# Kernel tuning notes

Measured on AMD Instinct MI355X. Metric: run time of the kernel, lower is better.

Reference implementation:

```python
import jax, jax.numpy as jnp
import numpy as np

WS = 7          # window size (square)
SHIFT = 3       # shift size
NH = 8          # num heads
DIM = 256
B, H, W = 32, 56, 56


def _relative_position_index(ws: int) -> np.ndarray:
    coords = np.stack(np.meshgrid(np.arange(ws), np.arange(ws), indexing='ij'))  # (2, ws, ws)
    cf = coords.reshape(2, -1)                                                   # (2, N)
    rel = cf[:, :, None] - cf[:, None, :]                                        # (2, N, N)
    rel = rel.transpose(1, 2, 0).copy()
    rel[:, :, 0] += ws - 1
    rel[:, :, 1] += ws - 1
    rel[:, :, 0] *= 2 * ws - 1
    return rel.sum(-1).reshape(-1).astype(np.int32)                              # (N*N,)


def _shift_mask(h: int, w: int, ws: int, shift: int) -> np.ndarray:
    img = np.zeros((h, w), dtype=np.float32)
    cnt = 0
    for hs in ((0, -ws), (-ws, -shift), (-shift, None)):
        for wsl in ((0, -ws), (-ws, -shift), (-shift, None)):
            img[hs[0]:hs[1], wsl[0]:wsl[1]] = cnt
            cnt += 1
    nwh, nww = h // ws, w // ws
    m = img.reshape(nwh, ws, nww, ws).transpose(0, 2, 1, 3).reshape(nwh * nww, ws * ws)
    am = m[:, None, :] - m[:, :, None]                 # (nW, N, N)
    return np.where(am != 0, np.float32(-100.0), np.float32(0.0))


def setup_inputs() -> dict:
    key = jax.random.key(0)
    ks = jax.random.split(key, 5)
    x = jax.random.normal(ks[0], (B, H, W, DIM), jnp.float32)
    qkv_weight = jax.random.normal(ks[1], (3 * DIM, DIM), jnp.float32) * 0.02
    qkv_bias = jnp.zeros((3 * DIM,), jnp.float32)
    proj_weight = jax.random.normal(ks[2], (DIM, DIM), jnp.float32) * 0.02
    proj_bias = jnp.zeros((DIM,), jnp.float32)
    rel_bias_table = jax.random.normal(ks[3], ((2 * WS - 1) ** 2, NH), jnp.float32) * 0.02
    rel_pos_index = jnp.asarray(_relative_position_index(WS))
    return {
        'x': x, 'qkv_weight': qkv_weight, 'qkv_bias': qkv_bias,
        'proj_weight': proj_weight, 'proj_bias': proj_bias,
        'rel_bias_table': rel_bias_table, 'rel_pos_index': rel_pos_index,
    }


def reference(x, qkv_weight, qkv_bias, proj_weight, proj_bias, rel_bias_table, rel_pos_index):
    b, h, w, c = x.shape
    n = WS * WS
    hd = c // NH
    nwh, nww = h // WS, w // WS
    nw = nwh * nww

    # relative position bias: (1, NH, N, N)
    bias = rel_bias_table[rel_pos_index].reshape(n, n, NH).transpose(2, 0, 1)[None]

    # cyclic shift
    xs = jnp.roll(x, (-SHIFT, -SHIFT), axis=(1, 2))

    # window partition -> (B*nW, N, C)
    xw = xs.reshape(b, nwh, WS, nww, WS, c).transpose(0, 1, 3, 2, 4, 5).reshape(b * nw, n, c)

    qkv = xw @ qkv_weight.T + qkv_bias
    qkv = qkv.reshape(b * nw, n, 3, NH, hd).transpose(2, 0, 3, 1, 4)  # (3, B*nW, NH, N, hd)
    q = qkv[0] * (hd ** -0.5)
    k = qkv[1]
    v = qkv[2]

    attn = jnp.einsum('bhnd,bhmd->bhnm', q, k) + bias                # (B*nW, NH, N, N)

    # shift mask (static)
    amask = jnp.asarray(_shift_mask(h, w, WS, SHIFT))                # (nW, N, N)
    attn = attn.reshape(b, nw, NH, n, n) + amask[None, :, None]
    attn = jax.nn.softmax(attn.reshape(b * nw, NH, n, n), axis=-1)

    out = jnp.einsum('bhnm,bhmd->bhnd', attn, v)                     # (B*nW, NH, N, hd)
    out = out.transpose(0, 2, 1, 3).reshape(b * nw, n, c)
    out = out @ proj_weight.T + proj_bias

    # window reverse + reverse shift
    out = out.reshape(b, nwh, nww, WS, WS, c).transpose(0, 1, 3, 2, 4, 5).reshape(b, h, w, c)
    out = jnp.roll(out, (SHIFT, SHIFT), axis=(1, 2))
    return out
```

## Files before the change

### kernel.cpp

```cpp
#include <hip/hip_runtime.h>
#include <hip/hip_bf16.h>


#define NTOK 49
#define DIM_ 256
#define NH_  8
#define NQKV 196608
#define NPRJ 65536
#define NTABP 131072

#define WSP_B  393216ull
#define TAB_B  524288ull
#define Q_B    1048576ull
#define NEED_BIG 162312448ull
#define NEED_TAB (TAB_B + (unsigned long long)NTABP * 4)

typedef short v8s __attribute__((ext_vector_type(8)));
typedef float v4f __attribute__((ext_vector_type(4)));
typedef float v16f __attribute__((ext_vector_type(16)));

#define MFMA16 __builtin_amdgcn_mfma_f32_16x16x32_bf16
#define MFMA32 __builtin_amdgcn_mfma_f32_32x32x16_bf16
#define LGKM_WAIT() asm volatile("s_waitcnt lgkmcnt(0)" ::: "memory")

static __device__ __forceinline__ v8s zero_v8s() {
    v8s z = {0, 0, 0, 0, 0, 0, 0, 0};
    return z;
}

static __device__ __forceinline__ v16f zero_v16f() {
    v16f z;
    #pragma unroll
    for (int i = 0; i < 16; ++i) z[i] = 0.0f;
    return z;
}

static __device__ __forceinline__ v8s lds_frag(const __hip_bfloat16* p, int row,
                                               int stride, int koff, int nrows) {
    if (row < nrows) return *(const v8s*)(p + row * stride + koff);
    return zero_v8s();
}

static __device__ __forceinline__ v8s cvt8(const float* p) {
    v4f a = *(const v4f*)p;
    v4f b = *(const v4f*)(p + 4);
    union { v8s v; __hip_bfloat16 h[8]; } r;
    r.h[0] = __float2bfloat16(a[0]); r.h[1] = __float2bfloat16(a[1]);
    r.h[2] = __float2bfloat16(a[2]); r.h[3] = __float2bfloat16(a[3]);
    r.h[4] = __float2bfloat16(b[0]); r.h[5] = __float2bfloat16(b[1]);
    r.h[6] = __float2bfloat16(b[2]); r.h[7] = __float2bfloat16(b[3]);
    return r.v;
}

__global__ __launch_bounds__(256) void prep_kernel(
    const float* __restrict__ qkvW, const float* __restrict__ projW,
    const float* __restrict__ rbt, const int* __restrict__ rpi,
    __hip_bfloat16* __restrict__ wsQ, __hip_bfloat16* __restrict__ wsP,
    float* __restrict__ tabP, int doTab)
{
    int i = blockIdx.x * 256 + threadIdx.x;
    if (i < NQKV) { wsQ[i] = __float2bfloat16(qkvW[i]); return; }
    int j = i - NQKV;
    if (j < NPRJ) { wsP[j] = __float2bfloat16(projW[j]); return; }
    int t = j - NPRJ;
    if (!doTab || t >= NTABP) return;
    int cls = t >> 15;
    int rem = t & 32767;
    int h = rem >> 12;
    int p = rem & 4095;
    int row = p >> 6, col = p & 63;
    float val = -1e30f;
    if (row < NTOK && col < NTOK) {
        int rh = (cls & 1) ? (((row / 7) < 4) ? 1 : 2) : 0;
        int rw = (cls & 2) ? (((row % 7) < 4) ? 1 : 2) : 0;
        int ch = (cls & 1) ? (((col / 7) < 4) ? 1 : 2) : 0;
        int cw = (cls & 2) ? (((col % 7) < 4) ? 1 : 2) : 0;
        float mask = ((rh * 3 + rw) != (ch * 3 + cw)) ? -100.0f : 0.0f;
        val = rbt[rpi[row * 49 + col] * NH_ + h] + mask;
    }
    tabP[t] = val;
}

__global__ __launch_bounds__(256) void qkvattn_kernel(
    const float* __restrict__ x,
    const float* __restrict__ qkvB,
    const __hip_bfloat16* __restrict__ wsQ,
    const float* __restrict__ tabP,
    __hip_bfloat16* __restrict__ OH)
{
    constexpr int SXS = 264;
    constexpr int QKS = 40;
    constexpr int VTS = 72;
    constexpr int PS  = 72;
    constexpr int WVSZ = 2 * NTOK * QKS + 32 * VTS;

    __shared__ alignas(16) __hip_bfloat16 s_x[NTOK * SXS];
    __shared__ alignas(16) __hip_bfloat16 s_wv[4 * WVSZ];

    const int tid = threadIdx.x, wave = tid >> 6, lane = tid & 63;
    const int quad = lane >> 4, l16 = lane & 15;
    const int l32 = lane & 31, half = lane >> 5;
    const int win = blockIdx.x;
    const int b = win >> 6, wh = (win >> 3) & 7, wwi = win & 7;
    const int cls = ((wh == 7) ? 1 : 0) | ((wwi == 7) ? 2 : 0);

    __hip_bfloat16* wq  = s_wv + wave * WVSZ;
    __hip_bfloat16* wk  = wq + NTOK * QKS;
    __hip_bfloat16* wvt = wq + 2 * NTOK * QKS;
    __hip_bfloat16* wp  = wq;

    for (int i = lane; i < 32 * 7; i += 64)
        wvt[(i / 7) * VTS + 49 + (i % 7)] = __float2bfloat16(0.0f);

    for (int i = tid; i < NTOK * 64; i += 256) {
        int tok = i >> 6, f4 = (i & 63) * 4;
        int r = tok / 7, c = tok - r * 7;
        int hg = wh * 7 + r + 3; if (hg >= 56) hg -= 56;
        int wg = wwi * 7 + c + 3; if (wg >= 56) wg -= 56;
        float4 v = *(const float4*)(x + ((b * 56 + hg) * 56 + wg) * DIM_ + f4);
        union { ushort4 u4; __hip_bfloat16 h[4]; } pkst;
        pkst.h[0] = __float2bfloat16(v.x);
        pkst.h[1] = __float2bfloat16(v.y);
        pkst.h[2] = __float2bfloat16(v.z);
        pkst.h[3] = __float2bfloat16(v.w);
        *(ushort4*)(s_x + tok * SXS + f4) = pkst.u4;
    }
    __syncthreads();

    const float qscale = 0.17677669529663687f;
    const int r1 = (32 + l32 < NTOK) ? (32 + l32) : 0;
    const __hip_bfloat16* arow0 = s_x + l32 * SXS + half * 8;
    const __hip_bfloat16* arow1 = s_x + r1 * SXS + half * 8;

    for (int hp = 0; hp < 2; ++hp) {
        const int h = wave * 2 + hp;

        #pragma unroll
        for (int m = 0; m < 3; ++m) {
            const int nb = m * 256 + h * 32;
            const __hip_bfloat16* wrow = wsQ + (nb + l32) * DIM_ + half * 8;
            v16f acc0 = zero_v16f(), acc1 = zero_v16f();

            if (m < 2) {
                #pragma unroll
                for (int kh = 0; kh < 2; ++kh) {
                    v8s wf[8];
                    #pragma unroll
                    for (int k = 0; k < 8; ++k)
                        wf[k] = *(const v8s*)(wrow + kh * 128 + k * 16);
                    #pragma unroll
                    for (int k = 0; k < 8; ++k) {
                        v8s a0 = *(const v8s*)(arow0 + kh * 128 + k * 16);
                        v8s a1 = *(const v8s*)(arow1 + kh * 128 + k * 16);
                        acc0 = MFMA32(a0, wf[k], acc0, 0, 0, 0);
                        acc1 = MFMA32(a1, wf[k], acc1, 0, 0, 0);
                    }
                }
                float bias = qkvB[nb + l32];
                float sc = (m == 0) ? qscale : 1.0f;
                __hip_bfloat16* dst = (m == 0) ? wq : wk;
                #pragma unroll
                for (int rg = 0; rg < 16; ++rg) {
                    int rowoff = (rg & 3) + 8 * (rg >> 2) + 4 * half;
                    dst[rowoff * QKS + l32] =
                        __float2bfloat16((acc0[rg] + bias) * sc);
                    int tok1 = 32 + rowoff;
                    if (tok1 < NTOK)
                        dst[tok1 * QKS + l32] =
                            __float2bfloat16((acc1[rg] + bias) * sc);
                }
            } else {
                #pragma unroll
                for (int kh = 0; kh < 2; ++kh) {
                    v8s wf[8];
                    #pragma unroll
                    for (int k = 0; k < 8; ++k)
                        wf[k] = *(const v8s*)(wrow + kh * 128 + k * 16);
                    #pragma unroll
                    for (int k = 0; k < 8; ++k) {
                        v8s b0 = *(const v8s*)(arow0 + kh * 128 + k * 16);
                        v8s b1 = *(const v8s*)(arow1 + kh * 128 + k * 16);
                        acc0 = MFMA32(wf[k], b0, acc0, 0, 0, 0);
                        acc1 = MFMA32(wf[k], b1, acc1, 0, 0, 0);
                    }
                }
                const int tok1 = 32 + l32;
                #pragma unroll
                for (int rg = 0; rg < 16; ++rg) {
                    int feat = (rg & 3) + 8 * (rg >> 2) + 4 * half;
                    float bias = qkvB[nb + feat];
                    wvt[feat * VTS + l32] = __float2bfloat16(acc0[rg] + bias);
                    if (tok1 < NTOK)
                        wvt[feat * VTS + tok1] = __float2bfloat16(acc1[rg] + bias);
                }
            }
        }
        LGKM_WAIT();

        const float* tabh = tabP + (cls * NH_ + h) * 4096;
        __hip_bfloat16* qs = OH + (win * NH_ + h) * (NTOK * 32);

        v8s qa[4], kb[4];
        #pragma unroll
        for (int mt = 0; mt < 4; ++mt) {
            qa[mt] = lds_frag(wq, mt * 16 + l16, QKS, quad * 8, NTOK);
            kb[mt] = lds_frag(wk, mt * 16 + l16, QKS, quad * 8, NTOK);
        }
        v8s pb[2][2];
        #pragma unroll
        for (int nt = 0; nt < 2; ++nt) {
            const __hip_bfloat16* vr = wvt + (nt * 16 + l16) * VTS;
            pb[nt][0] = *(const v8s*)(vr + quad * 8);
            pb[nt][1] = (quad == 3) ? zero_v8s() : *(const v8s*)(vr + 32 + quad * 8);
        }
        LGKM_WAIT();

        #pragma unroll
        for (int ntq = 0; ntq < 4; ++ntq) {
            const int qtok = ntq * 16 + l16;
            v4f tv[4];
            #pragma unroll
            for (int mt = 0; mt < 4; ++mt)
                tv[mt] = *(const v4f*)(tabh + qtok * 64 + mt * 16 + quad * 4);
            v4f st[4];
            #pragma unroll
            for (int mt = 0; mt < 4; ++mt) {
                v4f z = {0.f, 0.f, 0.f, 0.f};
                st[mt] = MFMA16(kb[mt], qa[ntq], z, 0, 0, 0);
            }
            float v[16];
            float rmax = -1e30f;
            #pragma unroll
            for (int mt = 0; mt < 4; ++mt)
                #pragma unroll
                for (int rg = 0; rg < 4; ++rg) {
                    float s = st[mt][rg] + tv[mt][rg];
                    v[mt * 4 + rg] = s;
                    rmax = fmaxf(rmax, s);
                }
            rmax = fmaxf(rmax, __shfl_xor(rmax, 16, 64));
            rmax = fmaxf(rmax, __shfl_xor(rmax, 32, 64));
            float rsum = 0.f;
            #pragma unroll
            for (int i = 0; i < 16; ++i) {
                float e = (v[i] <= -1e29f) ? 0.f : __expf(v[i] - rmax);
                v[i] = e;
                rsum += e;
            }
            rsum += __shfl_xor(rsum, 16, 64);
            rsum += __shfl_xor(rsum, 32, 64);
            if (qtok < NTOK) {
                float inv = 1.0f / rsum;
                #pragma unroll
                for (int mt = 0; mt < 4; ++mt) {
                    union { __hip_bfloat16 h4[4]; unsigned long long u; } pk;
                    #pragma unroll
                    for (int rg = 0; rg < 4; ++rg)
                        pk.h4[rg] = __float2bfloat16(v[mt * 4 + rg] * inv);
                    *(unsigned long long*)(wp + qtok * PS + mt * 16 + quad * 4) = pk.u;
                }
            }
        }
        LGKM_WAIT();

        #pragma unroll
        for (int mtile = 0; mtile < 4; ++mtile) {
            v8s pa0 = lds_frag(wp, mtile * 16 + l16, PS, quad * 8, NTOK);
            v8s pa1 = lds_frag(wp, mtile * 16 + l16, PS, 32 + quad * 8, NTOK);
            #pragma unroll
            for (int nt = 0; nt < 2; ++nt) {
                v4f z = {0.f, 0.f, 0.f, 0.f};
                v4f acc = MFMA16(pa0, pb[nt][0], z, 0, 0, 0);
                acc = MFMA16(pa1, pb[nt][1], acc, 0, 0, 0);
                #pragma unroll
                for (int rg = 0; rg < 4; ++rg) {
                    int tok = mtile * 16 + quad * 4 + rg;
                    if (tok < NTOK)
                        qs[tok * 32 + nt * 16 + l16] = __float2bfloat16(acc[rg]);
                }
            }
        }
        LGKM_WAIT();
    }
}

__global__ __launch_bounds__(256) void proj_kernel(
    const __hip_bfloat16* __restrict__ OH,
    const __hip_bfloat16* __restrict__ wsP,
    const float* __restrict__ projB,
    float* __restrict__ out)
{
    const int tid = threadIdx.x, wave = tid >> 6, lane = tid & 63;
    const int quad = lane >> 4, l16 = lane & 15;
    const int bid = blockIdx.x;
    const int win = (bid & 7) | ((bid >> 5) << 3);
    const int tq  = (bid >> 3) & 3;
    const int b = win >> 6, wh = (win >> 3) & 7, wwi = win & 7;
    const int m0 = wave * 16;
    const int tokA = m0 + l16;

    const __hip_bfloat16* ohw = OH + (size_t)win * (NH_ * NTOK * 32);
    v8s af[8];
    #pragma unroll
    for (int ks = 0; ks < 8; ++ks)
        af[ks] = (tokA < NTOK)
                   ? *(const v8s*)(ohw + ks * (NTOK * 32) + tokA * 32 + quad * 8)
                   : zero_v8s();

    int ooff[4];
    #pragma unroll
    for (int rg = 0; rg < 4; ++rg) {
        int row = m0 + quad * 4 + rg;
        if (row < NTOK) {
            int r = row / 7, c = row - r * 7;
            int hg = wh * 7 + r + 3; if (hg >= 56) hg -= 56;
            int wg = wwi * 7 + c + 3; if (wg >= 56) wg -= 56;
            ooff[rg] = ((b * 56 + hg) * 56 + wg) * DIM_;
        } else ooff[rg] = -1;
    }

    #pragma unroll
    for (int tt = 0; tt < 4; ++tt) {
        const int t = tq * 4 + tt;
        const __hip_bfloat16* wrow = wsP + (t * 16 + l16) * DIM_;
        v4f acc = {0.f, 0.f, 0.f, 0.f};
        #pragma unroll
        for (int ks = 0; ks < 8; ++ks) {
            v8s wf = *(const v8s*)(wrow + ks * 32 + quad * 8);
            acc = MFMA16(af[ks], wf, acc, 0, 0, 0);
        }
        float pbv = projB[t * 16 + l16];
        #pragma unroll
        for (int rg = 0; rg < 4; ++rg)
            if (ooff[rg] >= 0)
                out[ooff[rg] + t * 16 + l16] = acc[rg] + pbv;
    }
}

__global__ __launch_bounds__(256, 2) void swin_attn_fused(
    const float* __restrict__ x,
    const float* __restrict__ qkvB,
    const float* __restrict__ projB,
    const float* __restrict__ rbt,
    const int*   __restrict__ rpi,
    const __hip_bfloat16* __restrict__ wsQ,
    const __hip_bfloat16* __restrict__ wsP,
    const float* __restrict__ biasTab,
    float*       __restrict__ out)
{
    constexpr int QKS = 40;
    constexpr int VTS = 72;
    constexpr int PS  = 72;
    constexpr int OS  = 264;
    constexpr int WVSZ = 6224;

    __shared__ alignas(16) __hip_bfloat16 s_wv[4 * WVSZ];
    __shared__ alignas(16) __hip_bfloat16 s_o[NTOK * OS];
    __shared__ int s_off[NTOK];
    __shared__ int s_reg[NTOK];

    const int tid  = threadIdx.x;
    const int wave = tid >> 6;
    const int lane = tid & 63;
    const int quad = lane >> 4;
    const int l16  = lane & 15;

    const int wid  = blockIdx.x;
    const int b    = wid >> 6;
    const int wIdx = wid & 63;
    const int wh   = wIdx >> 3;
    const int wwi  = wIdx & 7;

    if (tid < NTOK) {
        int r = tid / 7, c = tid - r * 7;
        int hs = wh * 7 + r, ws = wwi * 7 + c;
        int hg = hs + 3; if (hg >= 56) hg -= 56;
        int wg = ws + 3; if (wg >= 56) wg -= 56;
        s_off[tid] = ((b * 56 + hg) * 56 + wg) * DIM_;
        int rh = (hs < 49) ? 0 : ((hs < 53) ? 1 : 2);
        int rw = (ws < 49) ? 0 : ((ws < 53) ? 1 : 2);
        s_reg[tid] = rh * 3 + rw;
    }

    __hip_bfloat16* wq  = s_wv + wave * WVSZ;
    __hip_bfloat16* wk  = wq + NTOK * QKS;
    __hip_bfloat16* wvt = wq + 2 * NTOK * QKS;
    __hip_bfloat16* wp  = wq;

    for (int i = lane; i < 32 * 15; i += 64) {
        int f = i / 15, kk = 49 + (i % 15);
        wvt[f * VTS + kk] = __float2bfloat16(0.0f);
    }
    __syncthreads();

    const float qscale = 0.17677669529663687f;

    for (int hp = 0; hp < 2; ++hp) {
        const int h = wave * 2 + hp;
        LGKM_WAIT();

        for (int mh = 0; mh < 2; ++mh) {
            const int mbase = mh * 32;
            v8s at[2][8];
            #pragma unroll
            for (int sub = 0; sub < 2; ++sub) {
                int tok = mbase + sub * 16 + l16;
                const float* xr = (tok < NTOK) ? (x + s_off[tok]) : nullptr;
                #pragma unroll
                for (int ks = 0; ks < 8; ++ks)
                    at[sub][ks] = xr ? cvt8(xr + ks * 32 + quad * 8) : zero_v8s();
            }
            #pragma unroll
            for (int t = 0; t < 6; ++t) {
                int mat = t >> 1, ntile = t & 1;
                int nout = mat * 256 + h * 32 + ntile * 16 + l16;
                const __hip_bfloat16* wrow = wsQ + nout * DIM_;
                v4f a0 = {0.f, 0.f, 0.f, 0.f}, a1 = {0.f, 0.f, 0.f, 0.f};
                #pragma unroll
                for (int ks = 0; ks < 8; ++ks) {
                    v8s bfr = *(const v8s*)(wrow + ks * 32 + quad * 8);
                    a0 = MFMA16(at[0][ks], bfr, a0, 0, 0, 0);
                    a1 = MFMA16(at[1][ks], bfr, a1, 0, 0, 0);
                }
                float bias  = qkvB[nout];
                float scale = (mat == 0) ? qscale : 1.0f;
                #pragma unroll
                for (int sub = 0; sub < 2; ++sub) {
                    v4f acc = sub ? a1 : a0;
                    #pragma unroll
                    for (int rg = 0; rg < 4; ++rg) {
                        int row = mbase + sub * 16 + quad * 4 + rg;
                        if (row < NTOK) {
                            float val = (acc[rg] + bias) * scale;
                            int col = ntile * 16 + l16;
                            __hip_bfloat16 bv = __float2bfloat16(val);
                            if (mat == 0)      wq[row * QKS + col] = bv;
                            else if (mat == 1) wk[row * QKS + col] = bv;
                            else               wvt[col * VTS + row] = bv;
                        }
                    }
                }
            }
        }
        LGKM_WAIT();

        v8s qa[4], kb[4];
        #pragma unroll
        for (int i = 0; i < 4; ++i) {
            qa[i] = lds_frag(wq, i * 16 + l16, QKS, quad * 8, NTOK);
            kb[i] = lds_frag(wk, i * 16 + l16, QKS, quad * 8, NTOK);
        }
        int regc[4];
        #pragma unroll
        for (int nt = 0; nt < 4; ++nt) {
            int col = nt * 16 + l16;
            regc[nt] = (col < NTOK) ? s_reg[col] : -1;
        }
        LGKM_WAIT();
        const float* tabh = biasTab ? (biasTab + h * 4096) : nullptr;
        #pragma unroll
        for (int mtile = 0; mtile < 4; ++mtile) {
            v4f sa[4];
            #pragma unroll
            for (int nt = 0; nt < 4; ++nt) {
                v4f z = {0.f, 0.f, 0.f, 0.f};
                sa[nt] = MFMA16(qa[mtile], kb[nt], z, 0, 0, 0);
            }
            #pragma unroll
            for (int rg = 0; rg < 4; ++rg) {
                int row = mtile * 16 + quad * 4 + rg;
                bool rok = row < NTOK;
                int rr = rok ? s_reg[row] : -2;
                float v[4];
                float rmax = -1e30f;
                #pragma unroll
                for (int nt = 0; nt < 4; ++nt) {
                    int col = nt * 16 + l16;
                    float s = -1e30f;
                    if (rok && col < NTOK) {
                        float bv = tabh ? tabh[row * 64 + col]
                                        : rbt[rpi[row * 49 + col] * NH_ + h];
                        s = sa[nt][rg] + bv;
                        if (rr != regc[nt]) s -= 100.0f;
                    }
                    v[nt] = s;
                    rmax = fmaxf(rmax, s);
                }
                #pragma unroll
                for (int mm = 8; mm >= 1; mm >>= 1)
                    rmax = fmaxf(rmax, __shfl_xor(rmax, mm, 64));
                float rsum = 0.f;
                #pragma unroll
                for (int nt = 0; nt < 4; ++nt) {
                    float e = (v[nt] <= -1e29f) ? 0.f : __expf(v[nt] - rmax);
                    v[nt] = e;
                    rsum += e;
                }
                #pragma unroll
                for (int mm = 8; mm >= 1; mm >>= 1)
                    rsum += __shfl_xor(rsum, mm, 64);
                if (rok) {
                    float inv = 1.0f / rsum;
                    #pragma unroll
                    for (int nt = 0; nt < 4; ++nt)
                        wp[row * PS + nt * 16 + l16] = __float2bfloat16(v[nt] * inv);
                }
            }
        }
        LGKM_WAIT();

        v8s pb[2][2];
        #pragma unroll
        for (int nt = 0; nt < 2; ++nt)
            #pragma unroll
            for (int ks = 0; ks < 2; ++ks)
                pb[nt][ks] = *(const v8s*)(wvt + (nt * 16 + l16) * VTS + ks * 32 + quad * 8);
        #pragma unroll
        for (int mtile = 0; mtile < 4; ++mtile) {
            v8s pa0 = lds_frag(wp, mtile * 16 + l16, PS, quad * 8, NTOK);
            v8s pa1 = lds_frag(wp, mtile * 16 + l16, PS, 32 + quad * 8, NTOK);
            #pragma unroll
            for (int nt = 0; nt < 2; ++nt) {
                v4f z = {0.f, 0.f, 0.f, 0.f};
                v4f acc = MFMA16(pa0, pb[nt][0], z, 0, 0, 0);
                acc = MFMA16(pa1, pb[nt][1], acc, 0, 0, 0);
                #pragma unroll
                for (int rg = 0; rg < 4; ++rg) {
                    int row = mtile * 16 + quad * 4 + rg;
                    if (row < NTOK)
                        s_o[row * OS + h * 32 + nt * 16 + l16] = __float2bfloat16(acc[rg]);
                }
            }
        }
    }
    __syncthreads();

    {
        int m0 = wave * 16;
        v8s af[8];
        #pragma unroll
        for (int ks = 0; ks < 8; ++ks)
            af[ks] = lds_frag(s_o, m0 + l16, OS, ks * 32 + quad * 8, NTOK);
        #pragma unroll
        for (int t = 0; t < 16; ++t) {
            const __hip_bfloat16* wrow = wsP + (t * 16 + l16) * DIM_;
            v4f acc = {0.f, 0.f, 0.f, 0.f};
            #pragma unroll
            for (int ks = 0; ks < 8; ++ks) {
                v8s bfr = *(const v8s*)(wrow + ks * 32 + quad * 8);
                acc = MFMA16(af[ks], bfr, acc, 0, 0, 0);
            }
            float pbv = projB[t * 16 + l16];
            #pragma unroll
            for (int rg = 0; rg < 4; ++rg) {
                int row = m0 + quad * 4 + rg;
                if (row < NTOK)
                    out[s_off[row] + t * 16 + l16] = acc[rg] + pbv;
            }
        }
    }
}

extern "C" void kernel_launch(void* const* d_in, const int* in_sizes, int n_in,
                              void* d_out, int out_size, void* d_ws, size_t ws_size,
                              hipStream_t stream) {
    const float* x     = (const float*)d_in[0];
    const float* qkvW  = (const float*)d_in[1];
    const float* qkvB  = (const float*)d_in[2];
    const float* projW = (const float*)d_in[3];
    const float* projB = (const float*)d_in[4];
    const float* rbt   = (const float*)d_in[5];
    const int*   rpi   = (const int*)d_in[6];
    float* o = (float*)d_out;

    __hip_bfloat16* wsQ = (__hip_bfloat16*)d_ws;
    __hip_bfloat16* wsP = (__hip_bfloat16*)((char*)d_ws + WSP_B);
    float* tabP         = (float*)((char*)d_ws + TAB_B);
    __hip_bfloat16* OH  = (__hip_bfloat16*)((char*)d_ws + Q_B);

    const int prepBlocks = (NQKV + NPRJ + NTABP + 255) / 256;

    if (ws_size >= NEED_BIG) {
        prep_kernel<<<prepBlocks, 256, 0, stream>>>(qkvW, projW, rbt, rpi,
                                                    wsQ, wsP, tabP, 1);
        qkvattn_kernel<<<2048, 256, 0, stream>>>(x, qkvB, wsQ, tabP, OH);
        proj_kernel<<<8192, 256, 0, stream>>>(OH, wsP, projB, o);
    } else {
        int doTab = (ws_size >= NEED_TAB) ? 1 : 0;
        prep_kernel<<<prepBlocks, 256, 0, stream>>>(qkvW, projW, rbt, rpi,
                                                    wsQ, wsP, tabP, doTab);
        swin_attn_fused<<<2048, 256, 0, stream>>>(x, qkvB, projB, rbt, rpi,
                                                  wsQ, wsP, doTab ? tabP : nullptr, o);
    }
}
```

Before: 467.0 us.

## Fuse QKV-attention and projection kernels into one per-window mega kernel

The separate projection kernel and the global bf16 head-output buffer are removed. Attention outputs now stay in registers across both head iterations, then go through shared memory, reusing the input tile buffer, and the output projection runs inside the same block. This drops the global round trip of the intermediate and one kernel launch. In exchange, register pressure rises from the extra accumulators. The projection also loses parallelism: 2048 blocks each do all 16 output tiles where the old kernel spread the work over 8192 blocks.

```diff
diff --git a/kernel.cpp b/kernel.cpp
--- a/kernel.cpp
+++ b/kernel.cpp
@@ -11,8 +11,6 @@
 
 #define WSP_B  393216ull
 #define TAB_B  524288ull
-#define Q_B    1048576ull
-#define NEED_BIG 162312448ull
 #define NEED_TAB (TAB_B + (unsigned long long)NTABP * 4)
 
 typedef short v8s __attribute__((ext_vector_type(8)));
@@ -81,12 +79,14 @@
     tabP[t] = val;
 }
 
-__global__ __launch_bounds__(256) void qkvattn_kernel(
+__global__ __launch_bounds__(256) void swin_mega_kernel(
     const float* __restrict__ x,
     const float* __restrict__ qkvB,
     const __hip_bfloat16* __restrict__ wsQ,
+    const __hip_bfloat16* __restrict__ wsP,
+    const float* __restrict__ projB,
     const float* __restrict__ tabP,
-    __hip_bfloat16* __restrict__ OH)
+    float* __restrict__ out)
 {
     constexpr int SXS = 264;
     constexpr int QKS = 40;
@@ -132,6 +132,9 @@
     const __hip_bfloat16* arow0 = s_x + l32 * SXS + half * 8;
     const __hip_bfloat16* arow1 = s_x + r1 * SXS + half * 8;
 
+    v4f ohacc[2][4][2];
+
+    #pragma unroll
     for (int hp = 0; hp < 2; ++hp) {
         const int h = wave * 2 + hp;
 
@@ -198,7 +201,6 @@
         LGKM_WAIT();
 
         const float* tabh = tabP + (cls * NH_ + h) * 4096;
-        __hip_bfloat16* qs = OH + (win * NH_ + h) * (NTOK * 32);
 
         v8s qa[4], kb[4];
         #pragma unroll
@@ -272,68 +274,67 @@
                 v4f z = {0.f, 0.f, 0.f, 0.f};
                 v4f acc = MFMA16(pa0, pb[nt][0], z, 0, 0, 0);
                 acc = MFMA16(pa1, pb[nt][1], acc, 0, 0, 0);
+                ohacc[hp][mtile][nt] = acc;
+            }
+        }
+        LGKM_WAIT();
+    }
+
+    __syncthreads();
+    __hip_bfloat16* s_o = s_x;
+
+    #pragma unroll
+    for (int hp = 0; hp < 2; ++hp) {
+        const int h = wave * 2 + hp;
+        #pragma unroll
+        for (int mtile = 0; mtile < 4; ++mtile)
+            #pragma unroll
+            for (int nt = 0; nt < 2; ++nt)
                 #pragma unroll
                 for (int rg = 0; rg < 4; ++rg) {
                     int tok = mtile * 16 + quad * 4 + rg;
                     if (tok < NTOK)
-                        qs[tok * 32 + nt * 16 + l16] = __float2bfloat16(acc[rg]);
-                }
-            }
-        }
-        LGKM_WAIT();
-    }
-}
-
-__global__ __launch_bounds__(256) void proj_kernel(
-    const __hip_bfloat16* __restrict__ OH,
-    const __hip_bfloat16* __restrict__ wsP,
-    const float* __restrict__ projB,
-    float* __restrict__ out)
-{
-    const int tid = threadIdx.x, wave = tid >> 6, lane = tid & 63;
-    const int quad = lane >> 4, l16 = lane & 15;
-    const int bid = blockIdx.x;
-    const int win = (bid & 7) | ((bid >> 5) << 3);
-    const int tq  = (bid >> 3) & 3;
-    const int b = win >> 6, wh = (win >> 3) & 7, wwi = win & 7;
-    const int m0 = wave * 16;
-    const int tokA = m0 + l16;
-
-    const __hip_bfloat16* ohw = OH + (size_t)win * (NH_ * NTOK * 32);
-    v8s af[8];
-    #pragma unroll
-    for (int ks = 0; ks < 8; ++ks)
-        af[ks] = (tokA < NTOK)
-                   ? *(const v8s*)(ohw + ks * (NTOK * 32) + tokA * 32 + quad * 8)
-                   : zero_v8s();
-
-    int ooff[4];
-    #pragma unroll
-    for (int rg = 0; rg < 4; ++rg) {
-        int row = m0 + quad * 4 + rg;
-        if (row < NTOK) {
-            int r = row / 7, c = row - r * 7;
-            int hg = wh * 7 + r + 3; if (hg >= 56) hg -= 56;
-            int wg = wwi * 7 + c + 3; if (wg >= 56) wg -= 56;
-            ooff[rg] = ((b * 56 + hg) * 56 + wg) * DIM_;
-        } else ooff[rg] = -1;
-    }
-
-    #pragma unroll
-    for (int tt = 0; tt < 4; ++tt) {
-        const int t = tq * 4 + tt;
-        const __hip_bfloat16* wrow = wsP + (t * 16 + l16) * DIM_;
-        v4f acc = {0.f, 0.f, 0.f, 0.f};
-        #pragma unroll
-        for (int ks = 0; ks < 8; ++ks) {
-            v8s wf = *(const v8s*)(wrow + ks * 32 + quad * 8);
-            acc = MFMA16(af[ks], wf, acc, 0, 0, 0);
-        }
-        float pbv = projB[t * 16 + l16];
-        #pragma unroll
-        for (int rg = 0; rg < 4; ++rg)
-            if (ooff[rg] >= 0)
-                out[ooff[rg] + t * 16 + l16] = acc[rg] + pbv;
+                        s_o[tok * SXS + h * 32 + nt * 16 + l16] =
+                            __float2bfloat16(ohacc[hp][mtile][nt][rg]);
+                }
+    }
+    __syncthreads();
+
+    {
+        const int m0 = wave * 16;
+        v8s af[8];
+        #pragma unroll
+        for (int ks = 0; ks < 8; ++ks)
+            af[ks] = lds_frag(s_o, m0 + l16, SXS, ks * 32 + quad * 8, NTOK);
+
+        int ooff[4];
+        #pragma unroll
+        for (int rg = 0; rg < 4; ++rg) {
+            int row = m0 + quad * 4 + rg;
+            if (row < NTOK) {
+                int r = row / 7, c = row - r * 7;
+                int hg = wh * 7 + r + 3; if (hg >= 56) hg -= 56;
+                int wg = wwi * 7 + c + 3; if (wg >= 56) wg -= 56;
+                ooff[rg] = ((b * 56 + hg) * 56 + wg) * DIM_;
+            } else ooff[rg] = -1;
+        }
+        LGKM_WAIT();
+
+        #pragma unroll
+        for (int t = 0; t < 16; ++t) {
+            const __hip_bfloat16* wrow = wsP + (t * 16 + l16) * DIM_;
+            v4f acc = {0.f, 0.f, 0.f, 0.f};
+            #pragma unroll
+            for (int ks = 0; ks < 8; ++ks) {
+                v8s wf = *(const v8s*)(wrow + ks * 32 + quad * 8);
+                acc = MFMA16(af[ks], wf, acc, 0, 0, 0);
+            }
+            float pbv = projB[t * 16 + l16];
+            #pragma unroll
+            for (int rg = 0; rg < 4; ++rg)
+                if (ooff[rg] >= 0)
+                    out[ooff[rg] + t * 16 + l16] = acc[rg] + pbv;
+        }
     }
 }
 
@@ -576,20 +577,18 @@
     __hip_bfloat16* wsQ = (__hip_bfloat16*)d_ws;
     __hip_bfloat16* wsP = (__hip_bfloat16*)((char*)d_ws + WSP_B);
     float* tabP         = (float*)((char*)d_ws + TAB_B);
-    __hip_bfloat16* OH  = (__hip_bfloat16*)((char*)d_ws + Q_B);
 
     const int prepBlocks = (NQKV + NPRJ + NTABP + 255) / 256;
 
-    if (ws_size >= NEED_BIG) {
+    if (ws_size >= NEED_TAB) {
         prep_kernel<<<prepBlocks, 256, 0, stream>>>(qkvW, projW, rbt, rpi,
                                                     wsQ, wsP, tabP, 1);
-        qkvattn_kernel<<<2048, 256, 0, stream>>>(x, qkvB, wsQ, tabP, OH);
-        proj_kernel<<<8192, 256, 0, stream>>>(OH, wsP, projB, o);
+        swin_mega_kernel<<<2048, 256, 0, stream>>>(x, qkvB, wsQ, wsP, projB,
+                                                   tabP, o);
     } else {
-        int doTab = (ws_size >= NEED_TAB) ? 1 : 0;
         prep_kernel<<<prepBlocks, 256, 0, stream>>>(qkvW, projW, rbt, rpi,
-                                                    wsQ, wsP, tabP, doTab);
+                                                    wsQ, wsP, tabP, 0);
         swin_attn_fused<<<2048, 256, 0, stream>>>(x, qkvB, projB, rbt, rpi,
-                                                  wsQ, wsP, doTab ? tabP : nullptr, o);
-    }
-}
+                                                  wsQ, wsP, nullptr, o);
+    }
+}
```

After: 437.2 us. 6.4% less time.
